# Optimization experiments

Hardware: AMD Instinct MI355X
Metric: run time of the kernel (lower is better)

The kernel has to match this reference:

```python
import jax, jax.numpy as jnp
import numpy as np

N = 16384   # total gate nodes (64 graphs x 256 gates)
B = 64      # graphs in batch
E = 49152   # directed edges (avg in-degree 3)
Q = 32      # qubit_num
F = 256     # feat_dim
D = 2 * F   # node feature dim = 512
H = 2       # heads
A = 128     # action_num


def _gatv2(x, wl, wr, att, b, src, dst, n):
    # PyG GATv2Conv (concat=True, share_weights=False, negative_slope=0.2)
    h, c = att.shape
    xl = (x @ wl).reshape(n, h, c)   # source-side projection [N,H,C]
    xr = (x @ wr).reshape(n, h, c)   # target-side projection [N,H,C]
    e = jax.nn.leaky_relu(xl[src] + xr[dst], 0.2)       # [E,H,C]
    logit = jnp.einsum('ehc,hc->eh', e, att)             # [E,H]
    m = jax.ops.segment_max(logit, dst, num_segments=n)  # softmax over in-edges per target
    p = jnp.exp(logit - m[dst])
    den = jax.ops.segment_sum(p, dst, num_segments=n)
    alpha = p / den[dst]                                 # [E,H]
    out = jax.ops.segment_sum(alpha[:, :, None] * xl[src], dst, num_segments=n)
    return out.reshape(n, h * c) + b


def _forward(x, xt_w1, xt_b1, xt_w2, xt_b2,
             g0_wl, g0_wr, g0_att, g0_b,
             g1_wl, g1_wr, g1_att, g1_b,
             g2_wl, g2_wr, g2_att, g2_b,
             g3_wl, g3_wr, g3_att, g3_b,
             g4_wl, g4_wr, g4_att, g4_b,
             ln_w, ln_b, aggr_t,
             m_w1, m_b1, m_w2, m_b2, m_w3, m_b3,
             edge_index, batch):
    lr = lambda v: jax.nn.leaky_relu(v, 0.01)
    # x_trans: Linear -> LeakyReLU -> Linear, then fold qubit-pairs into one node
    h0 = lr(x @ xt_w1 + xt_b1) @ xt_w2 + xt_b2           # [2N, F]
    cx = h0.reshape(-1, D)                               # [N, 2F]
    n = cx.shape[0]
    # GATv2Conv default add_self_loops=True (inputs contain no self loops)
    sl = jnp.arange(n, dtype=edge_index.dtype)
    src = jnp.concatenate([edge_index[0], sl])
    dst = jnp.concatenate([edge_index[1], sl])
    res = cx
    h = lr(_gatv2(cx, g0_wl, g0_wr, g0_att, g0_b, src, dst, n))
    for wl_, wr_, att_, b_ in ((g1_wl, g1_wr, g1_att, g1_b),
                               (g2_wl, g2_wr, g2_att, g2_b),
                               (g3_wl, g3_wr, g3_att, g3_b)):
        h = lr(_gatv2(h, wl_, wr_, att_, b_, src, dst, n))
    h = lr(_gatv2(h, g4_wl, g4_wr, g4_att, g4_b, src, dst, n))
    h = h + res                                           # residual [N, 2F]
    # PyG LayerNorm(mode='graph'): normalize over nodes AND channels per graph
    cnt = jax.ops.segment_sum(jnp.ones((n,), h.dtype), batch, num_segments=B)
    norm = cnt * h.shape[1]
    mean = jax.ops.segment_sum(h.sum(-1), batch, num_segments=B) / norm
    hc = h - mean[batch][:, None]
    var = jax.ops.segment_sum((hc * hc).sum(-1), batch, num_segments=B) / norm
    h = hc / jnp.sqrt(var + 1e-5)[batch][:, None] * ln_w + ln_b
    # SoftmaxAggregation(learn=True): channel-wise softmax over nodes per graph
    logit = h * aggr_t
    mg = jax.ops.segment_max(logit, batch, num_segments=B)
    p = jnp.exp(logit - mg[batch])
    den = jax.ops.segment_sum(p, batch, num_segments=B)
    g = jax.ops.segment_sum((p / den[batch]) * h, batch, num_segments=B)  # [B, 2F]
    # head MLP 512->384->256->128
    o = lr(g @ m_w1 + m_b1)
    o = lr(o @ m_w2 + m_b2)
    return o @ m_w3 + m_b3


def setup_inputs() -> dict:
    key = jax.random.key(0)
    ks = iter(jax.random.split(key, 64))
    def rn(shp, s=0.05):
        return jax.random.normal(next(ks), shp, jnp.float32) * s
    d = {}
    d['x'] = jax.random.normal(next(ks), (2 * N, Q), jnp.float32)
    src = jax.random.randint(next(ks), (E,), 0, N, jnp.int32)
    off = jax.random.randint(next(ks), (E,), 1, N, jnp.int32)
    d['edge_index'] = jnp.stack([src, (src + off) % N])  # no self loops
    d['batch'] = jnp.arange(N, dtype=jnp.int32) // (N // B)
    d['xt_w1'] = rn((Q, F)); d['xt_b1'] = rn((F,))
    d['xt_w2'] = rn((F, F)); d['xt_b2'] = rn((F,))
    d['g0_wl'] = rn((D, H * D)); d['g0_wr'] = rn((D, H * D))
    d['g0_att'] = rn((H, D));    d['g0_b'] = rn((H * D,))
    for i in (1, 2, 3):
        d[f'g{i}_wl'] = rn((H * D, H * D)); d[f'g{i}_wr'] = rn((H * D, H * D))
        d[f'g{i}_att'] = rn((H, D));        d[f'g{i}_b'] = rn((H * D,))
    d['g4_wl'] = rn((H * D, D)); d['g4_wr'] = rn((H * D, D))
    d['g4_att'] = rn((1, D));    d['g4_b'] = rn((D,))
    d['ln_w'] = jnp.ones((D,), jnp.float32); d['ln_b'] = jnp.zeros((D,), jnp.float32)
    d['aggr_t'] = jnp.array(1.0, jnp.float32)
    d['m_w1'] = rn((D, 384)); d['m_b1'] = rn((384,))
    d['m_w2'] = rn((384, 256)); d['m_b2'] = rn((256,))
    d['m_w3'] = rn((256, A)); d['m_b3'] = rn((A,))
    return d


def reference(x, edge_index, batch, xt_w1, xt_b1, xt_w2, xt_b2,
              g0_wl, g0_wr, g0_att, g0_b,
              g1_wl, g1_wr, g1_att, g1_b,
              g2_wl, g2_wr, g2_att, g2_b,
              g3_wl, g3_wr, g3_att, g3_b,
              g4_wl, g4_wr, g4_att, g4_b,
              ln_w, ln_b, aggr_t,
              m_w1, m_b1, m_w2, m_b2, m_w3, m_b3):
    return _forward(x, xt_w1, xt_b1, xt_w2, xt_b2,
                    g0_wl, g0_wr, g0_att, g0_b,
                    g1_wl, g1_wr, g1_att, g1_b,
                    g2_wl, g2_wr, g2_att, g2_b,
                    g3_wl, g3_wr, g3_att, g3_b,
                    g4_wl, g4_wr, g4_att, g4_b,
                    ln_w, ln_b, aggr_t,
                    m_w1, m_b1, m_w2, m_b2, m_w3, m_b3,
                    edge_index, batch)
```

## Files before the change

### kernel.cpp

```cpp
#include <hip/hip_runtime.h>
#include <hip/hip_bf16.h>

typedef __hip_bfloat16 bf16;

#define NN 16384
#define BBG 64
#define EE 49152
#define ET (EE + NN)
#define DD 512
#define NG (NN / BBG)

__device__ __forceinline__ float b2f(bf16 v) { return __bfloat162float(v); }
__device__ __forceinline__ bf16 f2b(float v) { return __float2bfloat16(v); }
__device__ __forceinline__ float sb2f(short s) {
    unsigned u = ((unsigned)(unsigned short)s) << 16;
    return __builtin_bit_cast(float, u);
}
__device__ __forceinline__ short f2bs(float v) {
    bf16 b = f2b(v);
    return __builtin_bit_cast(short, b);
}
__device__ __forceinline__ int clampi(int v, int lo, int hi)
{
    return v < lo ? lo : (v > hi ? hi : v);
}

typedef __attribute__((ext_vector_type(8))) short bf16x8;
typedef __attribute__((ext_vector_type(4))) float f32x4;

#define AS1 __attribute__((address_space(1)))
#define AS3 __attribute__((address_space(3)))

__device__ __forceinline__ int xcd_swizzle(int orig, int nwg)
{
    int q = nwg >> 3;
    int r = nwg & 7;
    int xcd = orig & 7;
    int idx = orig >> 3;
    return ((xcd < r) ? (xcd * (q + 1)) : (r * (q + 1) + (xcd - r) * q)) + idx;
}

__global__ __launch_bounds__(256) void gemm_mfma_bt(
    const bf16* __restrict__ A, const bf16* __restrict__ Bt,
    const float* __restrict__ bias, float* __restrict__ C,
    bf16* __restrict__ Cb, int M, int N, int K, float slope, int has_act)
{
    __shared__ bf16 As[128 * 32];
    __shared__ bf16 Bs[128 * 32];
    const int tid = threadIdx.x;
    const int w = tid >> 6;
    const int l = tid & 63;
    const int nwg = gridDim.x * gridDim.y;
    const int wg = xcd_swizzle(blockIdx.y * gridDim.x + blockIdx.x, nwg);
    const int bm = (wg / gridDim.x) * 128;
    const int bn = (wg % gridDim.x) * 128;
    const int wrow = (w >> 1) * 64;
    const int wcol = (w & 1) * 64;
    const int quad = l >> 4;
    const int c16 = l & 15;

    const int lrow = l >> 2;
    const int lchunk = l & 3;
    const bf16* Ag = A + (size_t)(bm + w * 16 + lrow) * K + lchunk * 8;
    const bf16* Bg = Bt + (size_t)(bn + w * 16 + lrow) * K + lchunk * 8;
    char* AsB = (char*)As;
    char* BsB = (char*)Bs;

    f32x4 acc[4][4] = {};

    for (int k0 = 0; k0 < K; k0 += 32) {
        __builtin_amdgcn_global_load_lds((const AS1 void*)(Ag + k0),
            (AS3 void*)(AsB + w * 1024), 16, 0, 0);
        __builtin_amdgcn_global_load_lds((const AS1 void*)(Ag + (size_t)64 * K + k0),
            (AS3 void*)(AsB + 4096 + w * 1024), 16, 0, 0);
        __builtin_amdgcn_global_load_lds((const AS1 void*)(Bg + k0),
            (AS3 void*)(BsB + w * 1024), 16, 0, 0);
        __builtin_amdgcn_global_load_lds((const AS1 void*)(Bg + (size_t)64 * K + k0),
            (AS3 void*)(BsB + 4096 + w * 1024), 16, 0, 0);
        __syncthreads();

        bf16x8 a[4], b[4];
#pragma unroll
        for (int i = 0; i < 4; i++) {
            int ra = wrow + i * 16 + c16;
            a[i] = *(const bf16x8*)(AsB + ra * 64 + quad * 16);
            int rb = wcol + i * 16 + c16;
            b[i] = *(const bf16x8*)(BsB + rb * 64 + quad * 16);
        }
#pragma unroll
        for (int i = 0; i < 4; i++)
#pragma unroll
            for (int j = 0; j < 4; j++)
                acc[i][j] = __builtin_amdgcn_mfma_f32_16x16x32_bf16(
                    a[i], b[j], acc[i][j], 0, 0, 0);
        __syncthreads();
    }

#pragma unroll
    for (int i = 0; i < 4; i++) {
#pragma unroll
        for (int j = 0; j < 4; j++) {
            int col = bn + wcol + j * 16 + c16;
            float bv = bias ? bias[col] : 0.f;
#pragma unroll
            for (int r = 0; r < 4; r++) {
                int row = bm + wrow + i * 16 + quad * 4 + r;
                float v = acc[i][j][r] + bv;
                if (has_act) v = (v >= 0.f) ? v : v * slope;
                if (C)  C[(size_t)row * N + col] = v;
                if (Cb) Cb[(size_t)row * N + col] = f2b(v);
            }
        }
    }
}

__global__ __launch_bounds__(256) void gemm_mfma_dual(
    const bf16* __restrict__ A, const bf16* __restrict__ Bt,
    bf16* __restrict__ X0, bf16* __restrict__ X1,
    int M, int Ntot, int K, int HC)
{
    __shared__ bf16 As[128 * 32];
    __shared__ bf16 Bs[128 * 32];
    const int tid = threadIdx.x;
    const int w = tid >> 6;
    const int l = tid & 63;
    const int nwg = gridDim.x * gridDim.y;
    const int wg = xcd_swizzle(blockIdx.y * gridDim.x + blockIdx.x, nwg);
    const int bm = (wg / gridDim.x) * 128;
    const int bn = (wg % gridDim.x) * 128;
    const int wrow = (w >> 1) * 64;
    const int wcol = (w & 1) * 64;
    const int quad = l >> 4;
    const int c16 = l & 15;

    const int lrow = l >> 2;
    const int lchunk = l & 3;
    const bf16* Ag = A + (size_t)(bm + w * 16 + lrow) * K + lchunk * 8;
    const bf16* Bg = Bt + (size_t)(bn + w * 16 + lrow) * K + lchunk * 8;
    char* AsB = (char*)As;
    char* BsB = (char*)Bs;

    f32x4 acc[4][4] = {};

    for (int k0 = 0; k0 < K; k0 += 32) {
        __builtin_amdgcn_global_load_lds((const AS1 void*)(Ag + k0),
            (AS3 void*)(AsB + w * 1024), 16, 0, 0);
        __builtin_amdgcn_global_load_lds((const AS1 void*)(Ag + (size_t)64 * K + k0),
            (AS3 void*)(AsB + 4096 + w * 1024), 16, 0, 0);
        __builtin_amdgcn_global_load_lds((const AS1 void*)(Bg + k0),
            (AS3 void*)(BsB + w * 1024), 16, 0, 0);
        __builtin_amdgcn_global_load_lds((const AS1 void*)(Bg + (size_t)64 * K + k0),
            (AS3 void*)(BsB + 4096 + w * 1024), 16, 0, 0);
        __syncthreads();

        bf16x8 a[4], b[4];
#pragma unroll
        for (int i = 0; i < 4; i++) {
            int ra = wrow + i * 16 + c16;
            a[i] = *(const bf16x8*)(AsB + ra * 64 + quad * 16);
            int rb = wcol + i * 16 + c16;
            b[i] = *(const bf16x8*)(BsB + rb * 64 + quad * 16);
        }
#pragma unroll
        for (int i = 0; i < 4; i++)
#pragma unroll
            for (int j = 0; j < 4; j++)
                acc[i][j] = __builtin_amdgcn_mfma_f32_16x16x32_bf16(
                    a[i], b[j], acc[i][j], 0, 0, 0);
        __syncthreads();
    }

#pragma unroll
    for (int i = 0; i < 4; i++) {
#pragma unroll
        for (int j = 0; j < 4; j++) {
            int col = bn + wcol + j * 16 + c16;
            bf16* dst = (col < HC) ? (X0 + col) : (X1 + col - HC);
#pragma unroll
            for (int r = 0; r < 4; r++) {
                int row = bm + wrow + i * 16 + quad * 4 + r;
                dst[(size_t)row * HC] = f2b(acc[i][j][r]);
            }
        }
    }
}

__global__ __launch_bounds__(256) void gemm_f32(
    const float* __restrict__ A, const float* __restrict__ W,
    const float* __restrict__ bias, float* __restrict__ C,
    int M, int N, int K, float slope, int has_act)
{
    const int BK = 16;
    __shared__ float Asm[BK][64 + 1];
    __shared__ float Wsm[BK][64 + 1];
    int tid = threadIdx.x;
    int bm = blockIdx.y * 64;
    int bn = blockIdx.x * 64;
    int tr = tid >> 4;
    int tc = tid & 15;
    float acc[4][4] = {};

    for (int k0 = 0; k0 < K; k0 += BK) {
        {
            int col = tid & 15;
            int row = tid >> 4;
#pragma unroll
            for (int p = 0; p < 4; p++) {
                int r = row + p * 16;
                Asm[col][r] = A[(size_t)(bm + r) * K + k0 + col];
            }
        }
        {
            int wc = tid & 63;
            int wr = tid >> 6;
#pragma unroll
            for (int p = 0; p < 4; p++) {
                int r = wr + p * 4;
                Wsm[r][wc] = W[(size_t)(k0 + r) * N + bn + wc];
            }
        }
        __syncthreads();
#pragma unroll
        for (int kk = 0; kk < BK; kk++) {
            float a[4], w[4];
#pragma unroll
            for (int i = 0; i < 4; i++) a[i] = Asm[kk][tr * 4 + i];
#pragma unroll
            for (int j = 0; j < 4; j++) w[j] = Wsm[kk][tc * 4 + j];
#pragma unroll
            for (int i = 0; i < 4; i++)
#pragma unroll
                for (int j = 0; j < 4; j++)
                    acc[i][j] += a[i] * w[j];
        }
        __syncthreads();
    }
#pragma unroll
    for (int i = 0; i < 4; i++) {
        int r = bm + tr * 4 + i;
#pragma unroll
        for (int j = 0; j < 4; j++) {
            int cn = bn + tc * 4 + j;
            float v = acc[i][j];
            if (bias) v += bias[cn];
            if (has_act) v = (v >= 0.f) ? v : v * slope;
            C[(size_t)r * N + cn] = v;
        }
    }
}

__global__ __launch_bounds__(256) void transpose_f2b2(
    const float* __restrict__ in0, bf16* __restrict__ out0,
    const float* __restrict__ in1, bf16* __restrict__ out1, int R, int C)
{
    const float* in = blockIdx.z ? in1 : in0;
    bf16* out = blockIdx.z ? out1 : out0;
    __shared__ float tile[32][33];
    int c0 = blockIdx.x * 32;
    int r0 = blockIdx.y * 32;
    int tx = threadIdx.x & 31;
    int ty = threadIdx.x >> 5;
#pragma unroll
    for (int k = 0; k < 4; k++) {
        int r = ty + k * 8;
        tile[r][tx] = in[(size_t)(r0 + r) * C + c0 + tx];
    }
    __syncthreads();
#pragma unroll
    for (int k = 0; k < 4; k++) {
        int rr = ty + k * 8;
        out[(size_t)(c0 + rr) * R + r0 + tx] = f2b(tile[tx][rr]);
    }
}

__global__ void f2b_vec(const float* __restrict__ in, bf16* __restrict__ out, int n)
{
    int i = blockIdx.x * 256 + threadIdx.x;
    if (i < n) out[i] = f2b(in[i]);
}

__global__ void count_deg(const int* __restrict__ ei, int* __restrict__ deg)
{
    int e = blockIdx.x * 256 + threadIdx.x;
    if (e >= ET) return;
    int d = (e < EE) ? ei[EE + e] : (e - EE);
    d = clampi(d, 0, NN - 1);
    atomicAdd(&deg[d], 1);
}

__global__ __launch_bounds__(256) void scan_deg(const int* __restrict__ deg,
                                                int* __restrict__ rs)
{
    __shared__ int part[256];
    __shared__ int psum[257];
    int tid = threadIdx.x;
    const int per = NN / 256;
    int base = tid * per;
    int s = 0;
    for (int i = 0; i < per; i++) s += deg[base + i];
    part[tid] = s;
    __syncthreads();
    if (tid == 0) {
        int acc = 0;
        for (int i = 0; i < 256; i++) { psum[i] = acc; acc += part[i]; }
        psum[256] = acc;
    }
    __syncthreads();
    int acc = psum[tid];
    for (int i = 0; i < per; i++) { rs[base + i] = acc; acc += deg[base + i]; }
    if (tid == 0) rs[NN] = psum[256];
}

__global__ void fill_csr(const int* __restrict__ ei, const int* __restrict__ rs,
                         int* __restrict__ cur, int* __restrict__ csrc)
{
    int e = blockIdx.x * 256 + threadIdx.x;
    if (e >= ET) return;
    int s, d;
    if (e < EE) { s = ei[e]; d = ei[EE + e]; } else { s = d = e - EE; }
    s = clampi(s, 0, NN - 1);
    d = clampi(d, 0, NN - 1);
    int pos = atomicAdd(&cur[d], 1);
    int slot = clampi(rs[d] + pos, 0, ET - 1);
    csrc[slot] = s;
}

template<int NH>
__global__ __launch_bounds__(256, 4) void gat_wave6(
    const bf16* __restrict__ xl, const bf16* __restrict__ xr,
    const float* __restrict__ att, const float* __restrict__ bias,
    const int* __restrict__ rs, const int* __restrict__ csrc,
    const float* __restrict__ res, float* __restrict__ out_f,
    bf16* __restrict__ out_b, float* __restrict__ lnsums)
{
    constexpr int HC = NH * 512;
    constexpr int PF = 6;
    constexpr int NODES = (NH == 2) ? 8 : 4;
    const int tid = threadIdx.x;
    const int w = tid >> 6;
    const int lane = tid & 63;
    const int wave_id = blockIdx.x * 4 + w;

    int msrc[NODES];
    int sdeg[NODES];
#pragma unroll
    for (int it = 0; it < NODES; ++it) {
        int gw = wave_id * NODES + it;
        int n = (NH == 2) ? (gw >> 1) : gw;
        int st = rs[n];
        int deg = clampi(rs[n + 1] - st, 1, 64);
        st = clampi(st, 0, ET - 1);
        st = __builtin_amdgcn_readfirstlane(st);
        deg = __builtin_amdgcn_readfirstlane(deg);
        sdeg[it] = deg;
        msrc[it] = csrc[st + ((lane < deg) ? lane : deg - 1)];
    }

    float av0[8], av1[8];
    {
        f32x4 t0 = *(const f32x4*)(att + lane * 8);
        f32x4 t1 = *(const f32x4*)(att + lane * 8 + 4);
#pragma unroll
        for (int k = 0; k < 4; k++) { av0[k] = t0[k]; av0[4 + k] = t1[k]; }
        if (NH == 2) {
            f32x4 t2 = *(const f32x4*)(att + 512 + lane * 8);
            f32x4 t3 = *(const f32x4*)(att + 512 + lane * 8 + 4);
#pragma unroll
            for (int k = 0; k < 4; k++) { av1[k] = t2[k]; av1[4 + k] = t3[k]; }
        } else {
#pragma unroll
            for (int k = 0; k < 8; k++) av1[k] = av0[k];
        }
    }

    f32x4 rows[2][PF];
    f32x4 rpx[2];

    auto issue = [&](int it, int pb) {
        int gw = wave_id * NODES + it;
        int n = (NH == 2) ? (gw >> 1) : gw;
        int h = (NH == 2) ? (gw & 1) : 0;
        int cb = h * 512 + lane * 8;
        rpx[pb] = *(const f32x4*)(xr + (size_t)n * HC + cb);
        int dm1 = sdeg[it] - 1;
#pragma unroll
        for (int r = 0; r < PF; r++) {
            int idx = (r < dm1) ? r : dm1;
            int s = __builtin_amdgcn_readlane(msrc[it], idx);
            s = clampi(s, 0, NN - 1);
            rows[pb][r] = *(const f32x4*)(xl + (size_t)s * HC + cb);
        }
    };

    auto compute = [&](int it, int pb) {
        int gw = wave_id * NODES + it;
        int n = (NH == 2) ? (gw >> 1) : gw;
        int h = (NH == 2) ? (gw & 1) : 0;
        int cb = h * 512 + lane * 8;
        int deg = sdeg[it];

        float rv[8], av[8];
        {
            bf16x8 xb = __builtin_bit_cast(bf16x8, rpx[pb]);
#pragma unroll
            for (int k = 0; k < 8; k++) {
                rv[k] = sb2f(xb[k]);
                av[k] = h ? av1[k] : av0[k];
            }
        }

        float part[PF];
#pragma unroll
        for (int r = 0; r < PF; r++) {
            bf16x8 rb = __builtin_bit_cast(bf16x8, rows[pb][r]);
            float p0 = 0.f, p1 = 0.f, p2 = 0.f, p3 = 0.f;
#pragma unroll
            for (int k = 0; k < 8; k += 4) {
                float x0 = sb2f(rb[k + 0]);
                float x1 = sb2f(rb[k + 1]);
                float x2 = sb2f(rb[k + 2]);
                float x3 = sb2f(rb[k + 3]);
                float u0 = x0 + rv[k + 0]; u0 = (u0 >= 0.f) ? u0 : 0.2f * u0;
                float u1 = x1 + rv[k + 1]; u1 = (u1 >= 0.f) ? u1 : 0.2f * u1;
                float u2 = x2 + rv[k + 2]; u2 = (u2 >= 0.f) ? u2 : 0.2f * u2;
                float u3 = x3 + rv[k + 3]; u3 = (u3 >= 0.f) ? u3 : 0.2f * u3;
                p0 = fmaf(av[k + 0], u0, p0);
                p1 = fmaf(av[k + 1], u1, p1);
                p2 = fmaf(av[k + 2], u2, p2);
                p3 = fmaf(av[k + 3], u3, p3);
            }
            part[r] = (p0 + p1) + (p2 + p3);
        }

#pragma unroll
        for (int msk = 32; msk; msk >>= 1) {
#pragma unroll
            for (int r = 0; r < PF; r++) part[r] += __shfl_xor(part[r], msk);
        }

        float m = -1e30f;
#pragma unroll
        for (int r = 0; r < PF; r++) {
            float vr = (r < deg) ? part[r] : -1e30f;
            m = fmaxf(m, vr);
        }
        float den = 0.f;
        float pw[PF];
#pragma unroll
        for (int r = 0; r < PF; r++) {
            float e = __expf(part[r] - m);
            pw[r] = (r < deg) ? e : 0.f;
            den += pw[r];
        }

        float acc[8];
#pragma unroll
        for (int k = 0; k < 8; k++) acc[k] = 0.f;
#pragma unroll
        for (int r = 0; r < PF; r++) {
            bf16x8 rb = __builtin_bit_cast(bf16x8, rows[pb][r]);
#pragma unroll
            for (int k = 0; k < 8; k++)
                acc[k] = fmaf(pw[r], sb2f(rb[k]), acc[k]);
        }

        if (deg > PF) {
            for (int i = PF; i < deg; i++) {
                int s = __builtin_amdgcn_readlane(msrc[it], i);
                s = clampi(s, 0, NN - 1);
                f32x4 rw = *(const f32x4*)(xl + (size_t)s * HC + cb);
                bf16x8 rb = __builtin_bit_cast(bf16x8, rw);
                float pt = 0.f;
#pragma unroll
                for (int k = 0; k < 8; k++) {
                    float x = sb2f(rb[k]);
                    float u = x + rv[k];
                    u = (u >= 0.f) ? u : 0.2f * u;
                    pt = fmaf(av[k], u, pt);
                }
#pragma unroll
                for (int msk = 32; msk; msk >>= 1) pt += __shfl_xor(pt, msk);
                float mn = fmaxf(m, pt);
                float rr = __expf(m - mn);
                float pi = __expf(pt - mn);
                m = mn;
                den = den * rr + pi;
#pragma unroll
                for (int k = 0; k < 8; k++) {
                    float x = sb2f(rb[k]);
                    acc[k] = fmaf(acc[k], rr, pi * x);
                }
            }
        }

        float inv = 1.f / den;
        f32x4 b0 = *(const f32x4*)(bias + cb);
        f32x4 b1 = *(const f32x4*)(bias + cb + 4);
        float vals[8];
#pragma unroll
        for (int k = 0; k < 8; k++) {
            float bv = (k < 4) ? b0[k] : b1[k - 4];
            float v = fmaf(acc[k], inv, bv);
            v = (v >= 0.f) ? v : 0.01f * v;
            vals[k] = v;
        }
        if (res) {
            float ls = 0.f, ls2 = 0.f;
#pragma unroll
            for (int k = 0; k < 8; k++) {
                vals[k] += res[(size_t)n * HC + cb + k];
                ls += vals[k];
                ls2 += vals[k] * vals[k];
            }
#pragma unroll
            for (int v = 0; v < 2; v++) {
                f32x4 ov;
#pragma unroll
                for (int k = 0; k < 4; k++) ov[k] = vals[v * 4 + k];
                *(f32x4*)(out_f + (size_t)n * HC + cb + v * 4) = ov;
            }
            if (lnsums) {
#pragma unroll
                for (int msk = 32; msk; msk >>= 1) {
                    ls += __shfl_xor(ls, msk);
                    ls2 += __shfl_xor(ls2, msk);
                }
                if (lane == 0) {
                    int g = n >> 8;
                    atomicAdd(&lnsums[g], ls);
                    atomicAdd(&lnsums[BBG + g], ls2);
                }
            }
        } else {
            bf16x8 ov;
#pragma unroll
            for (int k = 0; k < 8; k++) ov[k] = f2bs(vals[k]);
            *(bf16x8*)(out_b + (size_t)n * HC + cb) = ov;
        }
    };

    issue(0, 0);
#pragma unroll
    for (int it = 0; it < NODES; ++it) {
        int pb = it & 1;
        if (it + 1 < NODES) issue(it + 1, pb ^ 1);
        compute(it, pb);
    }
}

__global__ __launch_bounds__(256) void aggr_partial(
    const float* __restrict__ h, const float* __restrict__ lnsums,
    const float* __restrict__ lnw, const float* __restrict__ lnb,
    const float* __restrict__ t_, float* __restrict__ pm,
    float* __restrict__ pd, float* __restrict__ pa)
{
    int g = blockIdx.x, ch = blockIdx.y, nk = blockIdx.z;
    int tid = threadIdx.x;
    int c = ch * 256 + tid;
    const float tot = (float)(NG * DD);
    float S = lnsums[g], S2 = lnsums[BBG + g];
    float mu = S / tot;
    float iv = rsqrtf(fmaxf(S2 / tot - mu * mu, 0.f) + 1e-5f);
    float w = lnw[c], b = lnb[c], t = t_[0];
    size_t base = (size_t)g * NG * DD + (size_t)nk * 32 * DD + c;
    float m = -1e30f, den = 0.f, acc = 0.f;
    for (int i = 0; i < 32; i++) {
        float hn = (h[base + (size_t)i * DD] - mu) * iv * w + b;
        float lg = hn * t;
        if (lg > m) {
            float r = __expf(m - lg);
            den *= r; acc *= r; m = lg;
        }
        float p = __expf(lg - m);
        den += p; acc += p * hn;
    }
    size_t idx = (((size_t)g * 2 + ch) * 8 + nk) * 256 + tid;
    pm[idx] = m; pd[idx] = den; pa[idx] = acc;
}

__global__ __launch_bounds__(256) void aggr_combine(
    const float* __restrict__ pm, const float* __restrict__ pd,
    const float* __restrict__ pa, float* __restrict__ gout)
{
    int g = blockIdx.x, ch = blockIdx.y;
    int tid = threadIdx.x;
    size_t base = (((size_t)g * 2 + ch) * 8) * 256 + tid;
    float m = -1e30f;
#pragma unroll
    for (int k = 0; k < 8; k++) m = fmaxf(m, pm[base + k * 256]);
    float den = 0.f, acc = 0.f;
#pragma unroll
    for (int k = 0; k < 8; k++) {
        float r = __expf(pm[base + k * 256] - m);
        den += pd[base + k * 256] * r;
        acc += pa[base + k * 256] * r;
    }
    gout[(size_t)g * DD + ch * 256 + tid] = acc / den;
}

extern "C" void kernel_launch(void* const* d_in, const int* in_sizes, int n_in,
                              void* d_out, int out_size, void* d_ws, size_t ws_size,
                              hipStream_t stream)
{
    const float* x      = (const float*)d_in[0];
    const int*   ei     = (const int*)d_in[1];
    const float* xt_w1  = (const float*)d_in[3];
    const float* xt_b1  = (const float*)d_in[4];
    const float* xt_w2  = (const float*)d_in[5];
    const float* xt_b2  = (const float*)d_in[6];
    const float* ln_w   = (const float*)d_in[27];
    const float* ln_b   = (const float*)d_in[28];
    const float* aggr_t = (const float*)d_in[29];
    const float* m_w1   = (const float*)d_in[30];
    const float* m_b1   = (const float*)d_in[31];
    const float* m_w2   = (const float*)d_in[32];
    const float* m_b2   = (const float*)d_in[33];
    const float* m_w3   = (const float*)d_in[34];
    const float* m_b3   = (const float*)d_in[35];
    float* out = (float*)d_out;

    char* p = (char*)d_ws;
    auto take = [&](size_t bytes) {
        char* r = p;
        p += (bytes + 255) & ~(size_t)255;
        return r;
    };
    int* i_deg     = (int*)take((size_t)(NN + 1) * 4);
    int* i_rs      = (int*)take((size_t)(NN + 1) * 4);
    int* i_cur     = (int*)take((size_t)NN * 4);
    int* i_src     = (int*)take((size_t)ET * 4);
    float* f_sums  = (float*)take((size_t)2 * BBG * 4);
    float* f_pm    = (float*)take((size_t)BBG * 2 * 8 * 256 * 4);
    float* f_pd    = (float*)take((size_t)BBG * 2 * 8 * 256 * 4);
    float* f_pa    = (float*)take((size_t)BBG * 2 * 8 * 256 * 4);
    float* b_g     = (float*)take((size_t)BBG * DD * 4);
    float* b_m1    = (float*)take((size_t)BBG * 384 * 4);
    float* b_m2    = (float*)take((size_t)BBG * 256 * 4);
    float* b_res   = (float*)take((size_t)NN * DD * 4);
    float* b_h     = (float*)take((size_t)NN * DD * 4);
    bf16* b_resb   = (bf16*)take((size_t)NN * DD * 2);
    bf16* b_hb     = (bf16*)take((size_t)NN * 1024 * 2);
    bf16* b_xlb    = (bf16*)take((size_t)NN * 1024 * 2);
    bf16* b_xrb    = (bf16*)take((size_t)NN * 1024 * 2);
    bf16* b_xb     = (bf16*)take((size_t)2 * NN * 32 * 2);
    bf16* b_wcat   = (bf16*)take((size_t)2048 * 1024 * 2);
    bf16* b_w1b    = (bf16*)take((size_t)32 * 256 * 2);
    bf16* b_w2b    = (bf16*)take((size_t)256 * 256 * 2);
    bf16* b_t1b = b_hb;

    dim3 blk(256);

    hipMemsetAsync(i_deg, 0, (size_t)(NN + 1) * 4, stream);
    hipMemsetAsync(i_cur, 0, (size_t)NN * 4, stream);
    hipMemsetAsync(f_sums, 0, (size_t)2 * BBG * 4, stream);
    count_deg<<<ET / 256, blk, 0, stream>>>(ei, i_deg);
    scan_deg<<<1, blk, 0, stream>>>(i_deg, i_rs);
    fill_csr<<<ET / 256, blk, 0, stream>>>(ei, i_rs, i_cur, i_src);

    f2b_vec<<<(2 * NN * 32 + 255) / 256, blk, 0, stream>>>(x, b_xb, 2 * NN * 32);
    transpose_f2b2<<<dim3(256 / 32, 32 / 32, 1), blk, 0, stream>>>(
        xt_w1, b_w1b, xt_w1, b_w1b, 32, 256);
    transpose_f2b2<<<dim3(256 / 32, 256 / 32, 1), blk, 0, stream>>>(
        xt_w2, b_w2b, xt_w2, b_w2b, 256, 256);

    gemm_mfma_bt<<<dim3(256 / 128, 32768 / 128), blk, 0, stream>>>(
        b_xb, b_w1b, xt_b1, (float*)nullptr, b_t1b, 32768, 256, 32, 0.01f, 1);
    gemm_mfma_bt<<<dim3(256 / 128, 32768 / 128), blk, 0, stream>>>(
        b_t1b, b_w2b, xt_b2, b_res, b_resb, 32768, 256, 256, 0.f, 0);

    for (int L = 0; L < 5; L++) {
        const float* wl  = (const float*)d_in[7 + 4 * L];
        const float* wr  = (const float*)d_in[8 + 4 * L];
        const float* att = (const float*)d_in[9 + 4 * L];
        const float* gb  = (const float*)d_in[10 + 4 * L];
        int Fin = (L == 0) ? 512 : 1024;
        int HC  = (L == 4) ? 512 : 1024;
        const bf16* hin = (L == 0) ? b_resb : b_hb;

        transpose_f2b2<<<dim3(HC / 32, Fin / 32, 2), blk, 0, stream>>>(
            wl, b_wcat, wr, b_wcat + (size_t)HC * Fin, Fin, HC);
        gemm_mfma_dual<<<dim3(2 * HC / 128, NN / 128), blk, 0, stream>>>(
            hin, b_wcat, b_xlb, b_xrb, NN, 2 * HC, Fin, HC);
        if (L == 4) {
            gat_wave6<1><<<1024, blk, 0, stream>>>(
                b_xlb, b_xrb, att, gb, i_rs, i_src,
                b_res, b_h, (bf16*)nullptr, f_sums);
        } else {
            gat_wave6<2><<<1024, blk, 0, stream>>>(
                b_xlb, b_xrb, att, gb, i_rs, i_src,
                (const float*)nullptr, (float*)nullptr, b_hb, (float*)nullptr);
        }
    }

    aggr_partial<<<dim3(BBG, 2, 8), blk, 0, stream>>>(
        b_h, f_sums, ln_w, ln_b, aggr_t, f_pm, f_pd, f_pa);
    aggr_combine<<<dim3(BBG, 2), blk, 0, stream>>>(f_pm, f_pd, f_pa, b_g);

    gemm_f32<<<dim3(384 / 64, 1), blk, 0, stream>>>(
        b_g, m_w1, m_b1, b_m1, 64, 384, 512, 0.01f, 1);
    gemm_f32<<<dim3(256 / 64, 1), blk, 0, stream>>>(
        b_m1, m_w2, m_b2, b_m2, 64, 256, 384, 0.01f, 1);
    gemm_f32<<<dim3(128 / 64, 1), blk, 0, stream>>>(
        b_m2, m_w3, m_b3, out, 64, 128, 256, 0.f, 0);
}
```

Measured before the change: 1.107 ms.

## Split two-head GAT layers into logit, softmax and weighted-sum kernels

For the four two-head GATv2 layers, the single fused gat_wave6 kernel is replaced by three kernels. The first computes partial attention logits per 128-column slice, the second reduces the slices and computes the softmax numerators and denominators, and the third gathers xl rows weighted by alpha into the bf16 output. Splitting by column slice gives more blocks and parallelism per node, at the cost of reading xl twice and extra global traffic for intermediate logits. The XCD swizzle is also removed from both MFMA GEMMs in favour of plain block indexing.

```diff
diff --git a/kernel.cpp b/kernel.cpp
--- a/kernel.cpp
+++ b/kernel.cpp
@@ -31,15 +31,6 @@
 #define AS1 __attribute__((address_space(1)))
 #define AS3 __attribute__((address_space(3)))
 
-__device__ __forceinline__ int xcd_swizzle(int orig, int nwg)
-{
-    int q = nwg >> 3;
-    int r = nwg & 7;
-    int xcd = orig & 7;
-    int idx = orig >> 3;
-    return ((xcd < r) ? (xcd * (q + 1)) : (r * (q + 1) + (xcd - r) * q)) + idx;
-}
-
 __global__ __launch_bounds__(256) void gemm_mfma_bt(
     const bf16* __restrict__ A, const bf16* __restrict__ Bt,
     const float* __restrict__ bias, float* __restrict__ C,
@@ -50,10 +41,8 @@
     const int tid = threadIdx.x;
     const int w = tid >> 6;
     const int l = tid & 63;
-    const int nwg = gridDim.x * gridDim.y;
-    const int wg = xcd_swizzle(blockIdx.y * gridDim.x + blockIdx.x, nwg);
-    const int bm = (wg / gridDim.x) * 128;
-    const int bn = (wg % gridDim.x) * 128;
+    const int bm = blockIdx.y * 128;
+    const int bn = blockIdx.x * 128;
     const int wrow = (w >> 1) * 64;
     const int wcol = (w & 1) * 64;
     const int quad = l >> 4;
@@ -124,10 +113,8 @@
     const int tid = threadIdx.x;
     const int w = tid >> 6;
     const int l = tid & 63;
-    const int nwg = gridDim.x * gridDim.y;
-    const int wg = xcd_swizzle(blockIdx.y * gridDim.x + blockIdx.x, nwg);
-    const int bm = (wg / gridDim.x) * 128;
-    const int bn = (wg % gridDim.x) * 128;
+    const int bm = blockIdx.y * 128;
+    const int bn = blockIdx.x * 128;
     const int wrow = (w >> 1) * 64;
     const int wcol = (w & 1) * 64;
     const int quad = l >> 4;
@@ -323,6 +310,144 @@
     int pos = atomicAdd(&cur[d], 1);
     int slot = clampi(rs[d] + pos, 0, ET - 1);
     csrc[slot] = s;
+}
+
+
+__global__ __launch_bounds__(256) void gat_logit1024(
+    const bf16* __restrict__ xl, const bf16* __restrict__ xr,
+    const float* __restrict__ att,
+    const int* __restrict__ rs, const int* __restrict__ csrc,
+    float* __restrict__ pl)
+{
+    const int slice = blockIdx.x & 7;
+    const int chunk = blockIdx.x >> 3;
+    const int w = threadIdx.x >> 6;
+    const int lane = threadIdx.x & 63;
+    const int c0 = slice * 128 + lane * 2;
+    const float a0 = att[c0];
+    const float a1 = att[c0 + 1];
+    const int d0 = (chunk * 4 + w) * 16;
+
+    for (int di = 0; di < 16; ++di) {
+        int d = d0 + di;
+        int st = rs[d];
+        int de = clampi(rs[d + 1] - st, 1, 64);
+        st = __builtin_amdgcn_readfirstlane(clampi(st, 0, ET - 1));
+        de = __builtin_amdgcn_readfirstlane(de);
+        int msrc = csrc[st + ((lane < de) ? lane : de - 1)];
+        msrc = clampi(msrc, 0, NN - 1);
+        unsigned xrp = *(const unsigned*)(xr + (size_t)d * 1024 + c0);
+        float r0 = sb2f((short)(xrp & 0xffff));
+        float r1 = sb2f((short)(xrp >> 16));
+
+        for (int base = 0; base < de; base += 4) {
+            float part[4];
+#pragma unroll
+            for (int r = 0; r < 4; ++r) {
+                int idx = base + r;
+                if (idx > de - 1) idx = de - 1;
+                int s = __builtin_amdgcn_readlane(msrc, idx);
+                unsigned xp = *(const unsigned*)(xl + (size_t)s * 1024 + c0);
+                float x0 = sb2f((short)(xp & 0xffff));
+                float x1 = sb2f((short)(xp >> 16));
+                float u0 = x0 + r0; u0 = (u0 >= 0.f) ? u0 : 0.2f * u0;
+                float u1 = x1 + r1; u1 = (u1 >= 0.f) ? u1 : 0.2f * u1;
+                part[r] = fmaf(a0, u0, a1 * u1);
+            }
+#pragma unroll
+            for (int msk = 32; msk; msk >>= 1) {
+#pragma unroll
+                for (int r = 0; r < 4; ++r)
+                    part[r] += __shfl_xor(part[r], msk);
+            }
+            if (lane == 0) {
+#pragma unroll
+                for (int r = 0; r < 4; ++r)
+                    if (base + r < de)
+                        pl[(size_t)slice * ET + st + base + r] = part[r];
+            }
+        }
+    }
+}
+
+__global__ __launch_bounds__(256) void gat_alpha1024(
+    const float* __restrict__ pl, const int* __restrict__ rs,
+    float* __restrict__ al, float* __restrict__ dden)
+{
+    int d = blockIdx.x * 256 + threadIdx.x;
+    int st = rs[d];
+    int de = clampi(rs[d + 1] - st, 1, 64);
+    st = clampi(st, 0, ET - 1);
+#pragma unroll
+    for (int h = 0; h < 2; ++h) {
+        float m = -1e30f;
+        for (int i = 0; i < de; ++i) {
+            float l = 0.f;
+#pragma unroll
+            for (int s = 0; s < 4; ++s)
+                l += pl[(size_t)(h * 4 + s) * ET + st + i];
+            m = fmaxf(m, l);
+        }
+        float den = 0.f;
+        for (int i = 0; i < de; ++i) {
+            float l = 0.f;
+#pragma unroll
+            for (int s = 0; s < 4; ++s)
+                l += pl[(size_t)(h * 4 + s) * ET + st + i];
+            float p = __expf(l - m);
+            al[(size_t)h * ET + st + i] = p;
+            den += p;
+        }
+        dden[h * NN + d] = den;
+    }
+}
+
+__global__ __launch_bounds__(256) void gat_wsum1024(
+    const bf16* __restrict__ xl, const float* __restrict__ al,
+    const float* __restrict__ dden, const float* __restrict__ bias,
+    const int* __restrict__ rs, const int* __restrict__ csrc,
+    bf16* __restrict__ hb)
+{
+    const int slice = blockIdx.x & 7;
+    const int chunk = blockIdx.x >> 3;
+    const int h = slice >> 2;
+    const int w = threadIdx.x >> 6;
+    const int lane = threadIdx.x & 63;
+    const int c0 = slice * 128 + lane * 2;
+    const float b0 = bias[c0];
+    const float b1 = bias[c0 + 1];
+    const int d0 = (chunk * 4 + w) * 16;
+
+    for (int di = 0; di < 16; ++di) {
+        int d = d0 + di;
+        int st = rs[d];
+        int de = clampi(rs[d + 1] - st, 1, 64);
+        st = __builtin_amdgcn_readfirstlane(clampi(st, 0, ET - 1));
+        de = __builtin_amdgcn_readfirstlane(de);
+        int msrc = csrc[st + ((lane < de) ? lane : de - 1)];
+        msrc = clampi(msrc, 0, NN - 1);
+        float inv = 1.f / dden[h * NN + d];
+
+        float acc0 = 0.f, acc1 = 0.f;
+        for (int base = 0; base < de; base += 4) {
+#pragma unroll
+            for (int r = 0; r < 4; ++r) {
+                int idx = base + r;
+                bool ok = idx < de;
+                if (!ok) idx = de - 1;
+                int s = __builtin_amdgcn_readlane(msrc, idx);
+                float wgt = ok ? al[(size_t)h * ET + st + idx] : 0.f;
+                unsigned xp = *(const unsigned*)(xl + (size_t)s * 1024 + c0);
+                acc0 = fmaf(wgt, sb2f((short)(xp & 0xffff)), acc0);
+                acc1 = fmaf(wgt, sb2f((short)(xp >> 16)), acc1);
+            }
+        }
+        float v0 = fmaf(acc0, inv, b0); v0 = (v0 >= 0.f) ? v0 : 0.01f * v0;
+        float v1 = fmaf(acc1, inv, b1); v1 = (v1 >= 0.f) ? v1 : 0.01f * v1;
+        unsigned o = (unsigned)(unsigned short)f2bs(v0) |
+                     ((unsigned)(unsigned short)f2bs(v1) << 16);
+        *(unsigned*)(hb + (size_t)d * 1024 + c0) = o;
+    }
 }
 
 template<int NH>
@@ -633,6 +758,9 @@
     float* f_pm    = (float*)take((size_t)BBG * 2 * 8 * 256 * 4);
     float* f_pd    = (float*)take((size_t)BBG * 2 * 8 * 256 * 4);
     float* f_pa    = (float*)take((size_t)BBG * 2 * 8 * 256 * 4);
+    float* f_pl    = (float*)take((size_t)8 * ET * 4);
+    float* f_al    = (float*)take((size_t)2 * ET * 4);
+    float* f_dden  = (float*)take((size_t)2 * NN * 4);
     float* b_g     = (float*)take((size_t)BBG * DD * 4);
     float* b_m1    = (float*)take((size_t)BBG * 384 * 4);
     float* b_m2    = (float*)take((size_t)BBG * 256 * 4);
@@ -686,9 +814,12 @@
                 b_xlb, b_xrb, att, gb, i_rs, i_src,
                 b_res, b_h, (bf16*)nullptr, f_sums);
         } else {
-            gat_wave6<2><<<1024, blk, 0, stream>>>(
-                b_xlb, b_xrb, att, gb, i_rs, i_src,
-                (const float*)nullptr, (float*)nullptr, b_hb, (float*)nullptr);
+            gat_logit1024<<<2048, blk, 0, stream>>>(
+                b_xlb, b_xrb, att, i_rs, i_src, f_pl);
+            gat_alpha1024<<<NN / 256, blk, 0, stream>>>(
+                f_pl, i_rs, f_al, f_dden);
+            gat_wsum1024<<<2048, blk, 0, stream>>>(
+                b_xlb, f_al, f_dden, gb, i_rs, i_src, b_hb);
         }
     }
 
```

Measured after the change: 1.238 ms. +11.9%, slower.
